# Kernel optimization log

Measured on AMD Instinct MI355X. Metric: run time of the kernel, lower is better.

Reference implementation:

```python
import jax, jax.numpy as jnp
import numpy as np

BINS = 10
MOMENTUM = 0.5
N = 16_777_216  # flat element / class count


def setup_inputs() -> dict:
    key = jax.random.key(0)
    k1, k2 = jax.random.split(key)
    pred = jax.random.normal(k1, (N,), dtype=jnp.float32)
    target = jax.random.uniform(k2, (N,), dtype=jnp.float32)
    return {"pred": pred, "target": target}


def reference(pred, target):
    # edges = linspace(0,1,bins+1) with last edge nudged up by 1e-6
    edges = jnp.linspace(0.0, 1.0, BINS + 1).at[-1].add(1e-6)

    # gradient magnitude g = |sigmoid(pred).detach() - target|
    p_sig = jax.lax.stop_gradient(jax.nn.sigmoid(pred))
    g = jnp.abs(p_sig - target)

    valid = jnp.isfinite(g) & jnp.isfinite(target)
    total_samples = jnp.sum(valid).astype(jnp.float32)

    # torch.bucketize(g, edges) with right=False == searchsorted left
    inds = jnp.searchsorted(edges, g, side="left")  # values in [0, BINS]
    # bincount(inds, minlength=BINS) -> histogram over BINS+1 buckets,
    # counting only valid elements (scatter-add)
    sample_in_bin = jnp.zeros(BINS + 1, jnp.float32).at[inds].add(
        valid.astype(jnp.float32)
    )

    # EMA: stored acc_sum is never updated in the torch module (stays zeros),
    # so the local acc_sum = momentum*0 + (1-momentum)*counts each call.
    acc_sum_state = jnp.zeros(BINS + 1, jnp.float32)
    acc_sum = MOMENTUM * acc_sum_state + (1.0 - MOMENTUM) * sample_in_bin

    total_positives = jnp.sum(acc_sum)
    total_negatives = total_samples - total_positives  # computed pre-clamp
    total_positives = jnp.maximum(total_positives, 1.0)

    pred_det = jax.lax.stop_gradient(pred)
    ratio = total_negatives / total_positives
    weights = jnp.where(target > pred_det, ratio, 1.0)
    weights = jnp.where(valid, weights, 0.0)  # weights only defined on valid

    # F.cross_entropy with 1-D logits [C], float (soft-label) target [C],
    # per-class weight [C], reduction='mean' on a single unbatched sample:
    # loss = -sum_c w_c * t_c * log_softmax(pred)_c
    logp = jax.nn.log_softmax(pred)
    loss = -jnp.sum(weights * target * logp)
    return loss
```

## Files before the change

kernel.cpp:

```cpp
#include <hip/hip_runtime.h>
#include <math.h>


#define NT 256
#define UN 4
#define CHUNK_F4 (NT * UN)
#define NBLK 1024
#define SHIFTC 16.0f

typedef float vf4 __attribute__((ext_vector_type(4)));

__device__ __forceinline__ float min4(vf4 t) { return fminf(fminf(t.x, t.y), fminf(t.z, t.w)); }
__device__ __forceinline__ float max4(vf4 t) { return fmaxf(fmaxf(t.x, t.y), fmaxf(t.z, t.w)); }

struct Acc5 { float S, At, Bt, Agt, Bgt; };

__device__ __forceinline__ void acc_elem(Acc5& a, float p, float t) {
    const float L2E = 1.4426950408889634f;
    a.S += exp2f(fmaf(p, L2E, -SHIFTC));
    float ts = (t > p) ? t : 0.0f;
    a.Bt += t;
    a.Bgt += ts;
    a.At  = fmaf(t,  p, a.At);
    a.Agt = fmaf(ts, p, a.Agt);
}

__device__ __forceinline__ void acc_group(Acc5& a, vf4 p, vf4 t) {
    acc_elem(a, p.x, t.x); acc_elem(a, p.y, t.y);
    acc_elem(a, p.z, t.z); acc_elem(a, p.w, t.w);
}

__device__ __forceinline__ void hist_fix(float& hd, float p, float t) {
    const float L2E = 1.4426950408889634f;
    if (isfinite(t)) {
        float sig = 1.0f / (1.0f + exp2f(-p * L2E));
        float g = fabsf(sig - t);
        if (g > 1.000001f) hd += 1.0f;
    }
}

__device__ __forceinline__ void fix_group(float& hd, vf4 p, vf4 t) {
    hist_fix(hd, p.x, t.x); hist_fix(hd, p.y, t.y);
    hist_fix(hd, p.z, t.z); hist_fix(hd, p.w, t.w);
}

__device__ __forceinline__ void proc_group(Acc5& a, float& hd, vf4 P, vf4 T) {
    acc_group(a, P, T);
    if (!(min4(T) >= 0.0f && max4(T) <= 1.0f)) fix_group(hd, P, T);
}

#define LOAD_CHUNK(Pb, Tb, c)                                                   \
    do {                                                                        \
        int base_ = (c) * CHUNK_F4 + tid;                                       \
        _Pragma("unroll")                                                       \
        for (int u = 0; u < UN; u++)                                            \
            Pb[u] = __builtin_nontemporal_load(&p4[base_ + u * NT]);            \
        _Pragma("unroll")                                                       \
        for (int u = 0; u < UN; u++)                                            \
            Tb[u] = __builtin_nontemporal_load(&t4[base_ + u * NT]);            \
    } while (0)

#define PROC_CHUNK(Pb, Tb)                                                      \
    do {                                                                        \
        _Pragma("unroll")                                                       \
        for (int u = 0; u < UN; u++) proc_group(a, hd, Pb[u], Tb[u]);           \
    } while (0)

__device__ __forceinline__ void block_reduce_write(float* v, float* out8) {
    #pragma unroll
    for (int off = 32; off > 0; off >>= 1) {
        #pragma unroll
        for (int q = 0; q < 6; q++) v[q] += __shfl_down(v[q], off);
    }
    __shared__ float red[NT / 64][6];
    int wave = threadIdx.x >> 6;
    int lane = threadIdx.x & 63;
    if (lane == 0) {
        #pragma unroll
        for (int q = 0; q < 6; q++) red[wave][q] = v[q];
    }
    __syncthreads();
    if (threadIdx.x == 0) {
        float s[6];
        #pragma unroll
        for (int q = 0; q < 6; q++) s[q] = red[0][q];
        #pragma unroll
        for (int w = 1; w < NT / 64; w++)
            #pragma unroll
            for (int q = 0; q < 6; q++) s[q] += red[w][q];
        #pragma unroll
        for (int q = 0; q < 6; q++) out8[q] = s[q];
    }
}

__global__ __launch_bounds__(NT) void ghm_pass1(const float* __restrict__ pred,
                                                const float* __restrict__ targ,
                                                float* __restrict__ ws,
                                                int n, int nchunks) {
    const vf4* p4 = (const vf4*)pred;
    const vf4* t4 = (const vf4*)targ;
    int tid = threadIdx.x;
    int n4 = n >> 2;

    Acc5 a = {0.f, 0.f, 0.f, 0.f, 0.f};
    float hd = 0.0f;

    int cpb = nchunks / gridDim.x;
    int c0 = blockIdx.x * cpb;

    vf4 PA[UN], TA[UN], PB[UN], TB[UN];
    if (cpb > 0) {
        LOAD_CHUNK(PA, TA, c0);
        int k = 0;
        for (; k + 2 <= cpb; k += 2) {
            LOAD_CHUNK(PB, TB, c0 + k + 1);
            PROC_CHUNK(PA, TA);
            if (k + 2 < cpb) LOAD_CHUNK(PA, TA, c0 + k + 2);
            PROC_CHUNK(PB, TB);
        }
        if (k < cpb) PROC_CHUNK(PA, TA);
    }

    for (int c = gridDim.x * cpb + blockIdx.x; c < nchunks; c += gridDim.x) {
        LOAD_CHUNK(PA, TA, c);
        PROC_CHUNK(PA, TA);
    }

    for (int j = nchunks * CHUNK_F4 + blockIdx.x * NT + tid; j < n4;
         j += gridDim.x * NT) {
        vf4 P = __builtin_nontemporal_load(&p4[j]);
        vf4 T = __builtin_nontemporal_load(&t4[j]);
        proc_group(a, hd, P, T);
    }

    if (blockIdx.x == 0 && tid == 0) {
        for (int j = n4 << 2; j < n; j++) {
            float p = pred[j], t = targ[j];
            acc_elem(a, p, t);
            if (!(t >= 0.0f && t <= 1.0f)) hist_fix(hd, p, t);
        }
    }

    float v[6] = {a.S, a.At, a.Bt, a.Agt, a.Bgt, hd};
    block_reduce_write(v, &ws[(size_t)blockIdx.x * 8]);
}

__global__ __launch_bounds__(NT) void ghm_pass2(const float* __restrict__ ws,
                                                float* __restrict__ out, int nb, int n) {
    float v[6] = {0.f, 0.f, 0.f, 0.f, 0.f, 0.f};
    for (int i = threadIdx.x; i < nb; i += NT) {
        const float* p = &ws[(size_t)i * 8];
        #pragma unroll
        for (int q = 0; q < 6; q++) v[q] += p[q];
    }
    __shared__ float res[8];
    block_reduce_write(v, res);
    if (threadIdx.x == 0) {
        float S = res[0], At = res[1], Bt = res[2], Agt = res[3], Bgt = res[4], hd = res[5];
        float cnt  = (float)n;
        float hcnt = cnt - hd;
        float tp0  = 0.5f * hcnt;
        float tneg = cnt - tp0;
        float ratio = tneg / fmaxf(tp0, 1.0f);
        float A = ratio * Agt + (At - Agt);
        float B = ratio * Bgt + (Bt - Bgt);
        float lse = (log2f(S) + SHIFTC) * 0.69314718055994531f;
        out[0] = lse * B - A;
    }
}

extern "C" void kernel_launch(void* const* d_in, const int* in_sizes, int n_in,
                              void* d_out, int out_size, void* d_ws, size_t ws_size,
                              hipStream_t stream) {
    const float* pred = (const float*)d_in[0];
    const float* targ = (const float*)d_in[1];
    float* out = (float*)d_out;
    float* ws = (float*)d_ws;
    int n = in_sizes[0];
    int n4 = n >> 2;
    int nchunks = n4 / CHUNK_F4;

    int nb = NBLK;
    size_t cap = ws_size / (8 * sizeof(float));
    if ((size_t)nb > cap) nb = (int)cap;
    if (nb < 1) nb = 1;

    ghm_pass1<<<nb, NT, 0, stream>>>(pred, targ, ws, n, nchunks);
    ghm_pass2<<<1, NT, 0, stream>>>(ws, out, nb, n);
}
```

Baseline: 141.6 us.

## Deepen load pipeline to four rotating buffers with smaller chunks

Shrinks the per-chunk unroll from 4 to 2 float4 pairs and replaces double buffering with a four-stage rotating register pipeline, so three chunks of loads are in flight while one is processed. Loads of pred and target are interleaved. The aim is more memory-level parallelism per thread in this bandwidth-bound reduction. It keeps a similar register footprint, and falls back to a simple unpipelined loop when the chunks per block are not a multiple of 4.

```diff
diff --git a/kernel.cpp b/kernel.cpp
--- a/kernel.cpp
+++ b/kernel.cpp
@@ -3,7 +3,7 @@
 
 
 #define NT 256
-#define UN 4
+#define UN 2
 #define CHUNK_F4 (NT * UN)
 #define NBLK 1024
 #define SHIFTC 16.0f
@@ -49,21 +49,19 @@
     if (!(min4(T) >= 0.0f && max4(T) <= 1.0f)) fix_group(hd, P, T);
 }
 
-#define LOAD_CHUNK(Pb, Tb, c)                                                   \
+#define LOADC(Pb, Tb, c)                                                        \
     do {                                                                        \
         int base_ = (c) * CHUNK_F4 + tid;                                       \
-        _Pragma("unroll")                                                       \
-        for (int u = 0; u < UN; u++)                                            \
-            Pb[u] = __builtin_nontemporal_load(&p4[base_ + u * NT]);            \
-        _Pragma("unroll")                                                       \
-        for (int u = 0; u < UN; u++)                                            \
-            Tb[u] = __builtin_nontemporal_load(&t4[base_ + u * NT]);            \
+        Pb[0] = __builtin_nontemporal_load(&p4[base_]);                         \
+        Tb[0] = __builtin_nontemporal_load(&t4[base_]);                         \
+        Pb[1] = __builtin_nontemporal_load(&p4[base_ + NT]);                    \
+        Tb[1] = __builtin_nontemporal_load(&t4[base_ + NT]);                    \
     } while (0)
 
-#define PROC_CHUNK(Pb, Tb)                                                      \
+#define PROCC(Pb, Tb)                                                           \
     do {                                                                        \
-        _Pragma("unroll")                                                       \
-        for (int u = 0; u < UN; u++) proc_group(a, hd, Pb[u], Tb[u]);           \
+        proc_group(a, hd, Pb[0], Tb[0]);                                        \
+        proc_group(a, hd, Pb[1], Tb[1]);                                        \
     } while (0)
 
 __device__ __forceinline__ void block_reduce_write(float* v, float* out8) {
@@ -108,22 +106,32 @@
     int cpb = nchunks / gridDim.x;
     int c0 = blockIdx.x * cpb;
 
-    vf4 PA[UN], TA[UN], PB[UN], TB[UN];
-    if (cpb > 0) {
-        LOAD_CHUNK(PA, TA, c0);
+    vf4 P0[UN], T0[UN], P1[UN], T1[UN];
+    vf4 P2[UN], T2[UN], P3[UN], T3[UN];
+
+    if (cpb >= 4 && (cpb & 3) == 0) {
+        LOADC(P0, T0, c0);
+        LOADC(P1, T1, c0 + 1);
+        LOADC(P2, T2, c0 + 2);
         int k = 0;
-        for (; k + 2 <= cpb; k += 2) {
-            LOAD_CHUNK(PB, TB, c0 + k + 1);
-            PROC_CHUNK(PA, TA);
-            if (k + 2 < cpb) LOAD_CHUNK(PA, TA, c0 + k + 2);
-            PROC_CHUNK(PB, TB);
+        for (; k + 8 <= cpb; k += 4) {
+            LOADC(P3, T3, c0 + k + 3); PROCC(P0, T0);
+            LOADC(P0, T0, c0 + k + 4); PROCC(P1, T1);
+            LOADC(P1, T1, c0 + k + 5); PROCC(P2, T2);
+            LOADC(P2, T2, c0 + k + 6); PROCC(P3, T3);
         }
-        if (k < cpb) PROC_CHUNK(PA, TA);
+        LOADC(P3, T3, c0 + k + 3);
+        PROCC(P0, T0); PROCC(P1, T1); PROCC(P2, T2); PROCC(P3, T3);
+    } else {
+        for (int c = c0; c < c0 + cpb; c++) {
+            LOADC(P0, T0, c);
+            PROCC(P0, T0);
+        }
     }
 
     for (int c = gridDim.x * cpb + blockIdx.x; c < nchunks; c += gridDim.x) {
-        LOAD_CHUNK(PA, TA, c);
-        PROC_CHUNK(PA, TA);
+        LOADC(P0, T0, c);
+        PROCC(P0, T0);
     }
 
     for (int j = nchunks * CHUNK_F4 + blockIdx.x * NT + tid; j < n4;
```

Measured after the change: 139.4 us. About the same (-1.6%).
